# Kernel optimization log

Measured on AMD Instinct MI355X. Metric: run time of the kernel, lower is better.

Reference implementation:

```python
import jax, jax.numpy as jnp
import numpy as np

B, T, C, H = 2, 2048, 1024, 16
HD = C // H  # head dim = 64


def setup_inputs() -> dict:
    key = jax.random.key(0)
    ks = jax.random.split(key, 12)
    s = 1.0 / np.sqrt(C)
    return {
        "q": jax.random.normal(ks[0], (B, T, C), jnp.float32),
        "k": jax.random.normal(ks[1], (B, T, C), jnp.float32),
        "v": jax.random.normal(ks[2], (B, T, C), jnp.float32),
        "attn_bias": jax.random.normal(ks[3], (1, H, T, T), jnp.float32),
        "Wq": jax.random.normal(ks[4], (C, C), jnp.float32) * s,
        "bq": jnp.zeros((C,), jnp.float32),
        "Wk": jax.random.normal(ks[5], (C, C), jnp.float32) * s,
        "bk": jnp.zeros((C,), jnp.float32),
        "Wv": jax.random.normal(ks[6], (C, C), jnp.float32) * s,
        "bv": jnp.zeros((C,), jnp.float32),
        "Wp": jax.random.normal(ks[7], (C, C), jnp.float32) * s,
        "bp": jnp.zeros((C,), jnp.float32),
    }


def reference(q, k, v, attn_bias, Wq, bq, Wk, bk, Wv, bv, Wp, bp):
    # Linear projections (torch Linear: x @ W.T + b), then split heads -> [B,H,T,HD]
    def split_heads(x):
        return x.reshape(B, T, H, HD).transpose(0, 2, 1, 3)

    qh = split_heads(q @ Wq.T + bq)
    kh = split_heads(k @ Wk.T + bk)
    vh = split_heads(v @ Wv.T + bv)

    scale = 1.0 / np.sqrt(HD)
    att = jnp.einsum("bhqd,bhkd->bhqk", qh, kh) * scale  # [B,H,T,T]

    causal = jnp.tril(jnp.ones((T, T), dtype=bool))  # mask[:, :, -Tq:, :Tk]
    att_scores = jnp.where(causal[None, None], att, -jnp.inf)
    att_scores = att_scores + attn_bias

    att_probs = jax.nn.softmax(att_scores, axis=-1)
    y = jnp.einsum("bhqk,bhkd->bhqd", att_probs, vh)
    y = y.transpose(0, 2, 1, 3).reshape(B, T, C)
    y = y @ Wp.T + bp  # dropout p=0.0
    return (y, att_scores)
```

## Files before the change

### kernel.cpp

```cpp
#include <hip/hip_runtime.h>
#include <hip/hip_bf16.h>
#include <math.h>

#define B_ 2
#define T_ 2048
#define C_ 1024
#define H_ 16
#define HD_ 64
#define M_ (B_*T_)
#define K_ 1024

#define SCORE_NINF (-3.0e38f)

#define PART_BH 33792

typedef __attribute__((ext_vector_type(8))) short bf16x8;
typedef __attribute__((ext_vector_type(8))) unsigned short u16x8;
typedef __attribute__((ext_vector_type(4))) float f32x4;

__device__ __forceinline__ ushort f2bf_rne(float x) {
    union { float f; unsigned u; } c; c.f = x;
    unsigned r = c.u + 0x7fffu + ((c.u >> 16) & 1u);
    return (ushort)(r >> 16);
}
__device__ __forceinline__ float bfval(ushort h) {
    union { float f; unsigned u; } c; c.u = ((unsigned)h) << 16; return c.f;
}
__device__ __forceinline__ ushort bf16_hi(float x) {
    union { float f; unsigned u; } c; c.f = x; return (ushort)(c.u >> 16);
}
__device__ __forceinline__ void nt_store_f4(float* p, f32x4 v) {
    __builtin_nontemporal_store(v, (f32x4*)p);
}

__device__ __forceinline__ void gload_lds16(const void* g, void* l) {
    __builtin_amdgcn_global_load_lds(
        (const __attribute__((address_space(1))) unsigned int*)g,
        (__attribute__((address_space(3))) unsigned int*)l, 16, 0, 0);
}

__global__ __launch_bounds__(256) void split4_kernel(
    const float* __restrict__ W0, const float* __restrict__ W1,
    const float* __restrict__ W2, const float* __restrict__ W3,
    ushort* __restrict__ h0, ushort* __restrict__ l0,
    ushort* __restrict__ h1, ushort* __restrict__ l1,
    ushort* __restrict__ h2, ushort* __restrict__ l2,
    ushort* __restrict__ h3, ushort* __restrict__ l3)
{
    const int wsel = blockIdx.x >> 10;
    const float* src = (wsel == 0) ? W0 : (wsel == 1) ? W1 : (wsel == 2) ? W2 : W3;
    ushort* hi = (wsel == 0) ? h0 : (wsel == 1) ? h1 : (wsel == 2) ? h2 : h3;
    ushort* lo = (wsel == 0) ? l0 : (wsel == 1) ? l1 : (wsel == 2) ? l2 : l3;
    const int i = (((blockIdx.x & 1023) * 256) + threadIdx.x) * 4;
    const float4 x = *(const float4*)&src[i];
    ushort4 h, l;
    h.x = f2bf_rne(x.x); l.x = f2bf_rne(x.x - bfval(h.x));
    h.y = f2bf_rne(x.y); l.y = f2bf_rne(x.y - bfval(h.y));
    h.z = f2bf_rne(x.z); l.z = f2bf_rne(x.z - bfval(h.z));
    h.w = f2bf_rne(x.w); l.w = f2bf_rne(x.w - bfval(h.w));
    *(ushort4*)&hi[i] = h;
    *(ushort4*)&lo[i] = l;
}

__global__ __launch_bounds__(256) void gemm_qkv(
    const float* __restrict__ Xq, const float* __restrict__ Xk, const float* __restrict__ Xv,
    const ushort* __restrict__ Wqh, const ushort* __restrict__ Wql,
    const ushort* __restrict__ Wkh, const ushort* __restrict__ Wkl,
    const ushort* __restrict__ Wvh, const ushort* __restrict__ Wvl,
    const float* __restrict__ bq, const float* __restrict__ bk, const float* __restrict__ bv,
    ushort* __restrict__ qo_hi, ushort* __restrict__ qo_lo,
    ushort* __restrict__ ko_hi, ushort* __restrict__ ko_lo,
    ushort* __restrict__ vo_hi, ushort* __restrict__ vo_lo)
{
    constexpr int APITCH = 40;
    __shared__ ushort AhS[128 * APITCH];
    __shared__ ushort AlS[128 * APITCH];
    __shared__ ushort BhS[128 * 32];
    __shared__ ushort BlS[128 * 32];

    const int z = blockIdx.z;
    const float*  Xf = (z == 0) ? Xq : (z == 1) ? Xk : Xv;
    const ushort* Wh = (z == 0) ? Wqh : (z == 1) ? Wkh : Wvh;
    const ushort* Wl = (z == 0) ? Wql : (z == 1) ? Wkl : Wvl;
    const float*  bias = (z == 0) ? bq : (z == 1) ? bk : bv;
    ushort* out_hi = (z == 0) ? qo_hi : (z == 1) ? ko_hi : vo_hi;
    ushort* out_lo = (z == 0) ? qo_lo : (z == 1) ? ko_lo : vo_lo;

    const int tid  = threadIdx.x;
    const int lane = tid & 63;
    const int w    = tid >> 6;
    const int lr   = lane & 15, lk = lane >> 4;
    const int wr   = w >> 1,    wc = w & 1;
    const int bm   = blockIdx.x * 128;
    const int bn   = blockIdx.y * 128;

    f32x4 acc[4][4];
    #pragma unroll
    for (int i = 0; i < 4; ++i)
        #pragma unroll
        for (int j = 0; j < 4; ++j) acc[i][j] = (f32x4){0.f, 0.f, 0.f, 0.f};

    const int ar   = tid >> 1;
    const int aseg = (tid & 1) * 16;

    for (int k0 = 0; k0 < K_; k0 += 32) {
        {
            const int r0 = w * 32;
            #pragma unroll
            for (int ii = 0; ii < 2; ++ii) {
                const int rr = r0 + ii * 16;
                const size_t goff = (size_t)(bn + rr + (lane >> 2)) * K_ + k0 + (lane & 3) * 8;
                gload_lds16(Wh + goff, &BhS[rr * 32]);
                gload_lds16(Wl + goff, &BlS[rr * 32]);
            }
        }
        {
            const float* xp = Xf + (size_t)(bm + ar) * K_ + aseg + k0;
            const float4 f0 = *(const float4*)(xp + 0);
            const float4 f1 = *(const float4*)(xp + 4);
            const float4 f2 = *(const float4*)(xp + 8);
            const float4 f3 = *(const float4*)(xp + 12);
            float xs[16];
            xs[0]=f0.x; xs[1]=f0.y; xs[2]=f0.z; xs[3]=f0.w;
            xs[4]=f1.x; xs[5]=f1.y; xs[6]=f1.z; xs[7]=f1.w;
            xs[8]=f2.x; xs[9]=f2.y; xs[10]=f2.z; xs[11]=f2.w;
            xs[12]=f3.x; xs[13]=f3.y; xs[14]=f3.z; xs[15]=f3.w;
            u16x8 hv[2], lv[2];
            #pragma unroll
            for (int e = 0; e < 16; ++e) {
                const ushort hh = f2bf_rne(xs[e]);
                const ushort ll = f2bf_rne(xs[e] - bfval(hh));
                hv[e >> 3][e & 7] = hh;
                lv[e >> 3][e & 7] = ll;
            }
            *(u16x8*)&AhS[ar * APITCH + aseg]     = hv[0];
            *(u16x8*)&AhS[ar * APITCH + aseg + 8] = hv[1];
            *(u16x8*)&AlS[ar * APITCH + aseg]     = lv[0];
            *(u16x8*)&AlS[ar * APITCH + aseg + 8] = lv[1];
        }
        __syncthreads();

        bf16x8 afr[4][2], bfr[4][2];
        #pragma unroll
        for (int i = 0; i < 4; ++i) {
            const int arow = wr * 64 + i * 16 + lr;
            afr[i][0] = *(const bf16x8*)&AhS[arow * APITCH + lk * 8];
            afr[i][1] = *(const bf16x8*)&AlS[arow * APITCH + lk * 8];
        }
        #pragma unroll
        for (int j = 0; j < 4; ++j) {
            const int brow = wc * 64 + j * 16 + lr;
            bfr[j][0] = *(const bf16x8*)&BhS[brow * 32 + lk * 8];
            bfr[j][1] = *(const bf16x8*)&BlS[brow * 32 + lk * 8];
        }
        #pragma unroll
        for (int i = 0; i < 4; ++i)
            #pragma unroll
            for (int j = 0; j < 4; ++j) {
                acc[i][j] = __builtin_amdgcn_mfma_f32_16x16x32_bf16(afr[i][0], bfr[j][0], acc[i][j], 0, 0, 0);
                acc[i][j] = __builtin_amdgcn_mfma_f32_16x16x32_bf16(afr[i][0], bfr[j][1], acc[i][j], 0, 0, 0);
                acc[i][j] = __builtin_amdgcn_mfma_f32_16x16x32_bf16(afr[i][1], bfr[j][0], acc[i][j], 0, 0, 0);
            }
        __syncthreads();
    }

    const int m0 = bm + wr * 64;
    const int n0 = bn + wc * 64;
    #pragma unroll
    for (int j = 0; j < 4; ++j) {
        const int n = n0 + j * 16 + lr;
        const float bias_n = bias[n];
        #pragma unroll
        for (int i = 0; i < 4; ++i) {
            if (z == 2) {
                const int mbase = m0 + i * 16 + lk * 4;
                const int bb = mbase >> 11, t0 = mbase & 2047;
                const int hh = n >> 6, dd = n & 63;
                ushort4 h4, l4;
                float o;
                o = acc[i][j][0] + bias_n; h4.x = f2bf_rne(o); l4.x = f2bf_rne(o - bfval(h4.x));
                o = acc[i][j][1] + bias_n; h4.y = f2bf_rne(o); l4.y = f2bf_rne(o - bfval(h4.y));
                o = acc[i][j][2] + bias_n; h4.z = f2bf_rne(o); l4.z = f2bf_rne(o - bfval(h4.z));
                o = acc[i][j][3] + bias_n; h4.w = f2bf_rne(o); l4.w = f2bf_rne(o - bfval(h4.w));
                const size_t base = (((size_t)(bb * H_ + hh)) * HD_ + dd) * T_ + t0;
                *(ushort4*)&out_hi[base] = h4;
                *(ushort4*)&out_lo[base] = l4;
            } else {
                #pragma unroll
                for (int q = 0; q < 4; ++q) {
                    const int m = m0 + i * 16 + lk * 4 + q;
                    const float o = acc[i][j][q] + bias_n;
                    const int bb = m >> 11, tt = m & 2047;
                    const int hh = n >> 6, dd = n & 63;
                    const size_t idx = (((size_t)(bb * H_ + hh)) * T_ + tt) * HD_ + dd;
                    const ushort hv2 = f2bf_rne(o);
                    out_hi[idx] = hv2;
                    out_lo[idx] = f2bf_rne(o - bfval(hv2));
                }
            }
        }
    }
}

__global__ __launch_bounds__(256) void gemm_final(
    const ushort* __restrict__ Xh, const ushort* __restrict__ Xl,
    const ushort* __restrict__ Wh, const ushort* __restrict__ Wl,
    const float*  __restrict__ bias, float* __restrict__ outf)
{
    __shared__ ushort AhS[128 * 32];
    __shared__ ushort AlS[128 * 32];
    __shared__ ushort BhS[128 * 32];
    __shared__ ushort BlS[128 * 32];

    const int tid  = threadIdx.x;
    const int lane = tid & 63;
    const int w    = tid >> 6;
    const int lr   = lane & 15, lk = lane >> 4;
    const int wr   = w >> 1,    wc = w & 1;
    const int bm   = blockIdx.x * 128;
    const int bn   = blockIdx.y * 128;

    f32x4 acc[4][4];
    #pragma unroll
    for (int i = 0; i < 4; ++i)
        #pragma unroll
        for (int j = 0; j < 4; ++j) acc[i][j] = (f32x4){0.f, 0.f, 0.f, 0.f};

    for (int k0 = 0; k0 < K_; k0 += 32) {
        const int r0 = w * 32;
        #pragma unroll
        for (int ii = 0; ii < 2; ++ii) {
            const int rr = r0 + ii * 16;
            const size_t goffB = (size_t)(bn + rr + (lane >> 2)) * K_ + k0 + (lane & 3) * 8;
            gload_lds16(Wh + goffB, &BhS[rr * 32]);
            gload_lds16(Wl + goffB, &BlS[rr * 32]);
            const size_t goffA = (size_t)(bm + rr + (lane >> 2)) * K_ + k0 + (lane & 3) * 8;
            gload_lds16(Xh + goffA, &AhS[rr * 32]);
            gload_lds16(Xl + goffA, &AlS[rr * 32]);
        }
        __syncthreads();

        bf16x8 afr[4][2], bfr[4][2];
        #pragma unroll
        for (int i = 0; i < 4; ++i) {
            const int arow = wr * 64 + i * 16 + lr;
            afr[i][0] = *(const bf16x8*)&AhS[arow * 32 + lk * 8];
            afr[i][1] = *(const bf16x8*)&AlS[arow * 32 + lk * 8];
        }
        #pragma unroll
        for (int j = 0; j < 4; ++j) {
            const int brow = wc * 64 + j * 16 + lr;
            bfr[j][0] = *(const bf16x8*)&BhS[brow * 32 + lk * 8];
            bfr[j][1] = *(const bf16x8*)&BlS[brow * 32 + lk * 8];
        }
        #pragma unroll
        for (int i = 0; i < 4; ++i)
            #pragma unroll
            for (int j = 0; j < 4; ++j) {
                acc[i][j] = __builtin_amdgcn_mfma_f32_16x16x32_bf16(afr[i][0], bfr[j][0], acc[i][j], 0, 0, 0);
                acc[i][j] = __builtin_amdgcn_mfma_f32_16x16x32_bf16(afr[i][0], bfr[j][1], acc[i][j], 0, 0, 0);
                acc[i][j] = __builtin_amdgcn_mfma_f32_16x16x32_bf16(afr[i][1], bfr[j][0], acc[i][j], 0, 0, 0);
            }
        __syncthreads();
    }

    const int m0 = bm + wr * 64;
    const int n0 = bn + wc * 64;
    #pragma unroll
    for (int j = 0; j < 4; ++j) {
        const int n = n0 + j * 16 + lr;
        const float bias_n = bias[n];
        #pragma unroll
        for (int i = 0; i < 4; ++i)
            #pragma unroll
            for (int q = 0; q < 4; ++q)
                outf[(size_t)(m0 + i * 16 + lk * 4 + q) * C_ + n] = acc[i][j][q] + bias_n;
    }
}

#define SP 516

__global__ __launch_bounds__(256) void score_kernel(
    const ushort* __restrict__ q_hi, const ushort* __restrict__ q_lo,
    const ushort* __restrict__ k_hi, const ushort* __restrict__ k_lo,
    const float* __restrict__ bias,
    float* __restrict__ scores, float2* __restrict__ partials)
{
    __shared__ float biasT[16 * SP];
    __shared__ float scoreT[16 * SP];

    const int tid  = threadIdx.x;
    const int w    = tid >> 6, lane = tid & 63;
    const int lr   = lane & 15, lk = lane >> 4;

    const int h   = blockIdx.x >> 9;
    const int rem = blockIdx.x & 511;
    const int s   = rem >> 2;
    const int j   = rem & 3;
    const int qr0 = s * 16;
    const int ktmax = s >> 2;
    const int cbase = j * 512;
    const f32x4 ninf4 = (f32x4){SCORE_NINF, SCORE_NINF, SCORE_NINF, SCORE_NINF};

    if (j * 8 > ktmax) {
        #pragma unroll
        for (int b = 0; b < 2; ++b) {
            const size_t rbase = ((size_t)(b * 16 + h) * T_ + qr0);
            #pragma unroll
            for (int sw = 0; sw < 8; ++sw) {
                const int row = sw * 2 + (tid >> 7);
                const int col = (tid & 127) * 4;
                nt_store_f4(&scores[(rbase + row) * T_ + cbase + col], ninf4);
            }
        }
        return;
    }

    #pragma unroll
    for (int rr = 0; rr < 4; ++rr) {
        const int row = w * 4 + rr;
        const float* gsrc = bias + ((size_t)h * T_ + qr0 + row) * T_ + cbase + lane * 4;
        gload_lds16(gsrc,       &biasT[row * SP]);
        gload_lds16(gsrc + 256, &biasT[row * SP + 256]);
    }
    __syncthreads();

    const int qrow = qr0 + lr;
    #pragma unroll 1
    for (int b = 0; b < 2; ++b) {
        const int bh = b * 16 + h;
        const ushort* qhb = q_hi + (size_t)bh * T_ * HD_;
        const ushort* qlb = q_lo + (size_t)bh * T_ * HD_;
        const ushort* khb = k_hi + (size_t)bh * T_ * HD_;
        const ushort* klb = k_lo + (size_t)bh * T_ * HD_;
        float2* part_bh = partials + (size_t)bh * PART_BH;

        bf16x8 qf[2][2];
        #pragma unroll
        for (int s2 = 0; s2 < 2; ++s2) {
            const size_t qoff = (size_t)qrow * HD_ + s2 * 32 + lk * 8;
            qf[s2][0] = *(const bf16x8*)&qhb[qoff];
            qf[s2][1] = *(const bf16x8*)&qlb[qoff];
        }

        #pragma unroll
        for (int kk = 0; kk < 2; ++kk) {
            const int ktl = w * 2 + kk;
            const int kt  = j * 8 + ktl;
            const int lc0 = ktl * 64;
            if (kt > ktmax) {
                #pragma unroll
                for (int c = 0; c < 4; ++c)
                    *(f32x4*)&scoreT[lr * SP + lc0 + c * 16 + lk * 4] = ninf4;
                continue;
            }
            const int climit = (kt < ktmax) ? 4 : ((s & 3) + 1);
            f32x4 sc[4];
            #pragma unroll
            for (int c = 0; c < 4; ++c) {
                if (c < climit) {
                    f32x4 a = (f32x4){0.f, 0.f, 0.f, 0.f};
                    #pragma unroll
                    for (int s2 = 0; s2 < 2; ++s2) {
                        const size_t koff = (size_t)(kt * 64 + c * 16 + lr) * HD_ + s2 * 32 + lk * 8;
                        const bf16x8 kfh = *(const bf16x8*)&khb[koff];
                        const bf16x8 kfl = *(const bf16x8*)&klb[koff];
                        a = __builtin_amdgcn_mfma_f32_16x16x32_bf16(kfh, qf[s2][0], a, 0, 0, 0);
                        a = __builtin_amdgcn_mfma_f32_16x16x32_bf16(kfl, qf[s2][0], a, 0, 0, 0);
                        a = __builtin_amdgcn_mfma_f32_16x16x32_bf16(kfh, qf[s2][1], a, 0, 0, 0);
                    }
                    sc[c] = a;
                }
            }
            float tmax = SCORE_NINF;
            #pragma unroll
            for (int c = 0; c < 4; ++c) {
                const int loff = lr * SP + lc0 + c * 16 + lk * 4;
                if (c < climit) {
                    const f32x4 b4 = *(const f32x4*)&biasT[loff];
                    f32x4 o;
                    const int kc0 = kt * 64 + c * 16 + lk * 4;
                    #pragma unroll
                    for (int q4 = 0; q4 < 4; ++q4) {
                        const float sv = (kc0 + q4 <= qrow) ? sc[c][q4] * 0.125f + b4[q4]
                                                            : SCORE_NINF;
                        sc[c][q4] = sv;
                        tmax = fmaxf(tmax, sv);
                        o[q4] = sv;
                    }
                    *(f32x4*)&scoreT[loff] = o;
                } else {
                    *(f32x4*)&scoreT[loff] = ninf4;
                }
            }
            tmax = fmaxf(tmax, __shfl_xor(tmax, 16));
            tmax = fmaxf(tmax, __shfl_xor(tmax, 32));
            float tsum = 0.f;
            #pragma unroll
            for (int c = 0; c < 4; ++c) {
                if (c < climit) {
                    tsum += __expf(sc[c][0] - tmax);
                    tsum += __expf(sc[c][1] - tmax);
                    tsum += __expf(sc[c][2] - tmax);
                    tsum += __expf(sc[c][3] - tmax);
                }
            }
            tsum += __shfl_xor(tsum, 16);
            tsum += __shfl_xor(tsum, 32);
            if (lk == 0)
                part_bh[kt * (2080 - 32 * kt) + (qrow - kt * 64)] = make_float2(tmax, tsum);
        }
        __syncthreads();

        #pragma unroll
        for (int sw = 0; sw < 8; ++sw) {
            const int row = sw * 2 + (tid >> 7);
            const int col = (tid & 127) * 4;
            const f32x4 v = *(const f32x4*)&scoreT[row * SP + col];
            *(f32x4*)&scores[((size_t)bh * T_ + qr0 + row) * T_ + cbase + col] = v;
        }
        __syncthreads();
    }
}

__global__ __launch_bounds__(256) void reduce_kernel(
    const float2* __restrict__ partials, float2* __restrict__ ml)
{
    const int gid = blockIdx.x * 256 + threadIdx.x;
    const int bh = gid >> 11, r = gid & 2047;
    const float2* pb = partials + (size_t)bh * PART_BH;
    const int nt = (r >> 6) + 1;
    float M = SCORE_NINF;
    for (int t = 0; t < nt; ++t)
        M = fmaxf(M, pb[t * (2080 - 32 * t) + (r - (t << 6))].x);
    float L = 0.f;
    for (int t = 0; t < nt; ++t) {
        const float2 p = pb[t * (2080 - 32 * t) + (r - (t << 6))];
        L += p.y * __expf(p.x - M);
    }
    ml[gid] = make_float2(M, 1.f / L);
}

#define PVPITCH 260

__global__ __launch_bounds__(256) void pv_kernel(
    const ushort* __restrict__ vt_hi, const ushort* __restrict__ vt_lo,
    const float* __restrict__ scores, const float2* __restrict__ ml,
    ushort* __restrict__ y_hi, ushort* __restrict__ y_lo)
{
    __shared__ float stile[16 * PVPITCH];

    const int tid = threadIdx.x;
    const int w = tid >> 6, lane = tid & 63;
    const int lr = lane & 15, lk = lane >> 4;
    const int bh = 31 - ((int)blockIdx.x >> 6);
    const int p  = (int)blockIdx.x & 63;
    const int h = bh & 15, b = bh >> 4;

    const ushort* vhb = vt_hi + (size_t)bh * HD_ * T_;
    const ushort* vlb = vt_lo + (size_t)bh * HD_ * T_;

    #pragma unroll 1
    for (int half = 0; half < 2; ++half) {
        const int s = half ? (127 - p) : p;
        const int qr0 = s * 16;
        const int ktmax = s >> 2;
        const int nch = (ktmax + 4) >> 2;
        const float2 ml2 = ml[(size_t)bh * 2048 + qr0 + lr];
        const float M = ml2.x, invL = ml2.y;

        f32x4 yacc[4];
        #pragma unroll
        for (int c = 0; c < 4; ++c) yacc[c] = (f32x4){0.f, 0.f, 0.f, 0.f};

        #pragma unroll 1
        for (int ch = 0; ch < nch; ++ch) {
            const int cb = ch * 256;
            #pragma unroll
            for (int rr = 0; rr < 4; ++rr) {
                const int row = w * 4 + rr;
                const float* gsrc = scores + ((size_t)bh * T_ + qr0 + row) * T_ + cb + lane * 4;
                gload_lds16(gsrc, &stile[row * PVPITCH]);
            }
            __syncthreads();

            const int kt = ch * 4 + w;
            if (kt <= ktmax) {
                const int climit = (kt < ktmax) ? 4 : ((s & 3) + 1);
                const int s2max = (climit > 2) ? 2 : 1;
                bf16x8 pa[2][2];
                #pragma unroll
                for (int s2 = 0; s2 < 2; ++s2) {
                    if (s2 < s2max) {
                        const float* lsrc = &stile[lr * PVPITCH + w * 64 + s2 * 32 + lk * 8];
                        const f32x4 l0 = *(const f32x4*)(lsrc);
                        const f32x4 l1 = *(const f32x4*)(lsrc + 4);
                        float xs[8];
                        xs[0]=l0[0]; xs[1]=l0[1]; xs[2]=l0[2]; xs[3]=l0[3];
                        xs[4]=l1[0]; xs[5]=l1[1]; xs[6]=l1[2]; xs[7]=l1[3];
                        bf16x8 ph, pl;
                        #pragma unroll
                        for (int jj = 0; jj < 8; ++jj) {
                            const float pv = __expf(xs[jj] - M);
                            const ushort hv = bf16_hi(pv);
                            ph[jj] = (short)hv;
                            pl[jj] = (short)bf16_hi(pv - bfval(hv));
                        }
                        pa[s2][0] = ph;
                        pa[s2][1] = pl;
                    }
                }
                #pragma unroll
                for (int c2 = 0; c2 < 4; ++c2) {
                    #pragma unroll
                    for (int s2 = 0; s2 < 2; ++s2) {
                        if (s2 < s2max) {
                            const size_t voff = (size_t)(c2 * 16 + lr) * T_ + kt * 64 + s2 * 32 + lk * 8;
                            const bf16x8 vfh = *(const bf16x8*)&vhb[voff];
                            const bf16x8 vfl = *(const bf16x8*)&vlb[voff];
                            yacc[c2] = __builtin_amdgcn_mfma_f32_16x16x32_bf16(pa[s2][0], vfh, yacc[c2], 0, 0, 0);
                            yacc[c2] = __builtin_amdgcn_mfma_f32_16x16x32_bf16(pa[s2][0], vfl, yacc[c2], 0, 0, 0);
                            yacc[c2] = __builtin_amdgcn_mfma_f32_16x16x32_bf16(pa[s2][1], vfh, yacc[c2], 0, 0, 0);
                        }
                    }
                }
            }
            __syncthreads();
        }

        float* mbuf = stile;
        if (w > 0) {
            #pragma unroll
            for (int c2 = 0; c2 < 4; ++c2)
                *(f32x4*)&mbuf[((c2 * 3 + (w - 1)) * 64 + lane) * 4] = yacc[c2];
        }
        __syncthreads();
        if (w == 0) {
            float inv[4];
            #pragma unroll
            for (int q4 = 0; q4 < 4; ++q4) inv[q4] = __shfl(invL, lk * 4 + q4);
            #pragma unroll
            for (int c2 = 0; c2 < 4; ++c2) {
                f32x4 tot = yacc[c2];
                #pragma unroll
                for (int ww = 0; ww < 3; ++ww)
                    tot += *(const f32x4*)&mbuf[((c2 * 3 + ww) * 64 + lane) * 4];
                #pragma unroll
                for (int q4 = 0; q4 < 4; ++q4) {
                    const int yr = qr0 + lk * 4 + q4;
                    const float val = tot[q4] * inv[q4];
                    const size_t yi = ((size_t)b * T_ + yr) * C_ + h * HD_ + c2 * 16 + lr;
                    const ushort hv = f2bf_rne(val);
                    y_hi[yi] = hv;
                    y_lo[yi] = f2bf_rne(val - bfval(hv));
                }
            }
        }
        __syncthreads();
    }
}

extern "C" void kernel_launch(void* const* d_in, const int* in_sizes, int n_in,
                              void* d_out, int out_size, void* d_ws, size_t ws_size,
                              hipStream_t stream) {
    const float* q         = (const float*)d_in[0];
    const float* k         = (const float*)d_in[1];
    const float* v         = (const float*)d_in[2];
    const float* attn_bias = (const float*)d_in[3];
    const float* Wq        = (const float*)d_in[4];
    const float* bq        = (const float*)d_in[5];
    const float* Wk        = (const float*)d_in[6];
    const float* bk        = (const float*)d_in[7];
    const float* Wv        = (const float*)d_in[8];
    const float* bv        = (const float*)d_in[9];
    const float* Wp        = (const float*)d_in[10];
    const float* bp        = (const float*)d_in[11];

    float* y_out      = (float*)d_out;
    float* scores_out = y_out + (size_t)B_*T_*C_;

    ushort* ws = (ushort*)d_ws;
    const size_t NE = (size_t)B_*H_*T_*HD_;
    const size_t WN = (size_t)C_*K_;
    ushort* q_hi  = ws + 0*NE;
    ushort* q_lo  = ws + 1*NE;
    ushort* k_hi  = ws + 2*NE;
    ushort* k_lo  = ws + 3*NE;
    ushort* vt_hi = ws + 4*NE;
    ushort* vt_lo = ws + 5*NE;
    ushort* Wph   = ws + 6*NE;
    ushort* Wpl   = Wph + WN;
    ushort* Wqh   = Wpl + WN;
    ushort* Wql   = Wqh + WN;
    ushort* Wkh   = Wql + WN;
    ushort* Wkl   = Wkh + WN;
    ushort* Wvh   = Wkl + WN;
    ushort* Wvl   = Wvh + WN;
    float2* partials = (float2*)(ws + 6*NE + 2*WN);
    float2* ml    = (float2*)(ws + 0*NE);
    ushort* y_hi  = ws + 1*NE;
    ushort* y_lo  = ws + 2*NE;

    split4_kernel<<<4096, 256, 0, stream>>>(Wq, Wk, Wv, Wp,
        Wqh, Wql, Wkh, Wkl, Wvh, Wvl, Wph, Wpl);

    gemm_qkv<<<dim3(M_/128, C_/128, 3), 256, 0, stream>>>(
        q, k, v, Wqh, Wql, Wkh, Wkl, Wvh, Wvl, bq, bk, bv,
        q_hi, q_lo, k_hi, k_lo, vt_hi, vt_lo);

    score_kernel<<<8192, 256, 0, stream>>>(q_hi, q_lo, k_hi, k_lo, attn_bias,
                                           scores_out, partials);
    reduce_kernel<<<256, 256, 0, stream>>>(partials, ml);
    pv_kernel<<<2048, 256, 0, stream>>>(vt_hi, vt_lo, scores_out, ml, y_hi, y_lo);

    gemm_final<<<dim3(M_/128, C_/128), 256, 0, stream>>>(
        y_hi, y_lo, Wph, Wpl, bp, y_out);
}
```

Baseline: 706.6 us.

## Split score kernel blocks per batch and merge bias and score LDS tiles

Each score block now handles a single batch index, so the grid doubles and the in-block batch loop is gone. Adjacent blocks (b=0,1) share the same attention-bias tile, so the reuse moves from inside one block to the L2 cache. One LDS tile holds the bias and is overwritten with scores, which halves shared memory per block and should raise occupancy. In exchange the bias is loaded from global memory twice instead of once per block, and there are more block launches.

```diff
diff --git a/kernel.cpp b/kernel.cpp
--- a/kernel.cpp
+++ b/kernel.cpp
@@ -286,17 +286,18 @@
     const float* __restrict__ bias,
     float* __restrict__ scores, float2* __restrict__ partials)
 {
-    __shared__ float biasT[16 * SP];
-    __shared__ float scoreT[16 * SP];
+    __shared__ float tile[16 * SP];
 
     const int tid  = threadIdx.x;
     const int w    = tid >> 6, lane = tid & 63;
     const int lr   = lane & 15, lk = lane >> 4;
 
-    const int h   = blockIdx.x >> 9;
-    const int rem = blockIdx.x & 511;
-    const int s   = rem >> 2;
-    const int j   = rem & 3;
+    const int bid = blockIdx.x;
+    const int b   = bid & 1;
+    const int j   = (bid >> 1) & 3;
+    const int s   = (bid >> 3) & 127;
+    const int h   = bid >> 10;
+    const int bh  = b * 16 + h;
     const int qr0 = s * 16;
     const int ktmax = s >> 2;
     const int cbase = j * 512;
@@ -304,14 +305,10 @@
 
     if (j * 8 > ktmax) {
         #pragma unroll
-        for (int b = 0; b < 2; ++b) {
-            const size_t rbase = ((size_t)(b * 16 + h) * T_ + qr0);
-            #pragma unroll
-            for (int sw = 0; sw < 8; ++sw) {
-                const int row = sw * 2 + (tid >> 7);
-                const int col = (tid & 127) * 4;
-                nt_store_f4(&scores[(rbase + row) * T_ + cbase + col], ninf4);
-            }
+        for (int sw = 0; sw < 8; ++sw) {
+            const int row = sw * 2 + (tid >> 7);
+            const int col = (tid & 127) * 4;
+            nt_store_f4(&scores[((size_t)bh * T_ + qr0 + row) * T_ + cbase + col], ninf4);
         }
         return;
     }
@@ -320,106 +317,101 @@
     for (int rr = 0; rr < 4; ++rr) {
         const int row = w * 4 + rr;
         const float* gsrc = bias + ((size_t)h * T_ + qr0 + row) * T_ + cbase + lane * 4;
-        gload_lds16(gsrc,       &biasT[row * SP]);
-        gload_lds16(gsrc + 256, &biasT[row * SP + 256]);
+        gload_lds16(gsrc,       &tile[row * SP]);
+        gload_lds16(gsrc + 256, &tile[row * SP + 256]);
     }
     __syncthreads();
 
     const int qrow = qr0 + lr;
-    #pragma unroll 1
-    for (int b = 0; b < 2; ++b) {
-        const int bh = b * 16 + h;
-        const ushort* qhb = q_hi + (size_t)bh * T_ * HD_;
-        const ushort* qlb = q_lo + (size_t)bh * T_ * HD_;
-        const ushort* khb = k_hi + (size_t)bh * T_ * HD_;
-        const ushort* klb = k_lo + (size_t)bh * T_ * HD_;
-        float2* part_bh = partials + (size_t)bh * PART_BH;
-
-        bf16x8 qf[2][2];
-        #pragma unroll
-        for (int s2 = 0; s2 < 2; ++s2) {
-            const size_t qoff = (size_t)qrow * HD_ + s2 * 32 + lk * 8;
-            qf[s2][0] = *(const bf16x8*)&qhb[qoff];
-            qf[s2][1] = *(const bf16x8*)&qlb[qoff];
-        }
-
-        #pragma unroll
-        for (int kk = 0; kk < 2; ++kk) {
-            const int ktl = w * 2 + kk;
-            const int kt  = j * 8 + ktl;
-            const int lc0 = ktl * 64;
-            if (kt > ktmax) {
+    const ushort* qhb = q_hi + (size_t)bh * T_ * HD_;
+    const ushort* qlb = q_lo + (size_t)bh * T_ * HD_;
+    const ushort* khb = k_hi + (size_t)bh * T_ * HD_;
+    const ushort* klb = k_lo + (size_t)bh * T_ * HD_;
+    float2* part_bh = partials + (size_t)bh * PART_BH;
+
+    bf16x8 qf[2][2];
+    #pragma unroll
+    for (int s2 = 0; s2 < 2; ++s2) {
+        const size_t qoff = (size_t)qrow * HD_ + s2 * 32 + lk * 8;
+        qf[s2][0] = *(const bf16x8*)&qhb[qoff];
+        qf[s2][1] = *(const bf16x8*)&qlb[qoff];
+    }
+
+    #pragma unroll
+    for (int kk = 0; kk < 2; ++kk) {
+        const int ktl = w * 2 + kk;
+        const int kt  = j * 8 + ktl;
+        const int lc0 = ktl * 64;
+        if (kt > ktmax) {
+            #pragma unroll
+            for (int c = 0; c < 4; ++c)
+                *(f32x4*)&tile[lr * SP + lc0 + c * 16 + lk * 4] = ninf4;
+            continue;
+        }
+        const int climit = (kt < ktmax) ? 4 : ((s & 3) + 1);
+        f32x4 sc[4];
+        #pragma unroll
+        for (int c = 0; c < 4; ++c) {
+            if (c < climit) {
+                f32x4 a = (f32x4){0.f, 0.f, 0.f, 0.f};
                 #pragma unroll
-                for (int c = 0; c < 4; ++c)
-                    *(f32x4*)&scoreT[lr * SP + lc0 + c * 16 + lk * 4] = ninf4;
-                continue;
-            }
-            const int climit = (kt < ktmax) ? 4 : ((s & 3) + 1);
-            f32x4 sc[4];
-            #pragma unroll
-            for (int c = 0; c < 4; ++c) {
-                if (c < climit) {
-                    f32x4 a = (f32x4){0.f, 0.f, 0.f, 0.f};
-                    #pragma unroll
-                    for (int s2 = 0; s2 < 2; ++s2) {
-                        const size_t koff = (size_t)(kt * 64 + c * 16 + lr) * HD_ + s2 * 32 + lk * 8;
-                        const bf16x8 kfh = *(const bf16x8*)&khb[koff];
-                        const bf16x8 kfl = *(const bf16x8*)&klb[koff];
-                        a = __builtin_amdgcn_mfma_f32_16x16x32_bf16(kfh, qf[s2][0], a, 0, 0, 0);
-                        a = __builtin_amdgcn_mfma_f32_16x16x32_bf16(kfl, qf[s2][0], a, 0, 0, 0);
-                        a = __builtin_amdgcn_mfma_f32_16x16x32_bf16(kfh, qf[s2][1], a, 0, 0, 0);
-                    }
-                    sc[c] = a;
+                for (int s2 = 0; s2 < 2; ++s2) {
+                    const size_t koff = (size_t)(kt * 64 + c * 16 + lr) * HD_ + s2 * 32 + lk * 8;
+                    const bf16x8 kfh = *(const bf16x8*)&khb[koff];
+                    const bf16x8 kfl = *(const bf16x8*)&klb[koff];
+                    a = __builtin_amdgcn_mfma_f32_16x16x32_bf16(kfh, qf[s2][0], a, 0, 0, 0);
+                    a = __builtin_amdgcn_mfma_f32_16x16x32_bf16(kfl, qf[s2][0], a, 0, 0, 0);
+                    a = __builtin_amdgcn_mfma_f32_16x16x32_bf16(kfh, qf[s2][1], a, 0, 0, 0);
                 }
-            }
-            float tmax = SCORE_NINF;
-            #pragma unroll
-            for (int c = 0; c < 4; ++c) {
-                const int loff = lr * SP + lc0 + c * 16 + lk * 4;
-                if (c < climit) {
-                    const f32x4 b4 = *(const f32x4*)&biasT[loff];
-                    f32x4 o;
-                    const int kc0 = kt * 64 + c * 16 + lk * 4;
-                    #pragma unroll
-                    for (int q4 = 0; q4 < 4; ++q4) {
-                        const float sv = (kc0 + q4 <= qrow) ? sc[c][q4] * 0.125f + b4[q4]
-                                                            : SCORE_NINF;
-                        sc[c][q4] = sv;
-                        tmax = fmaxf(tmax, sv);
-                        o[q4] = sv;
-                    }
-                    *(f32x4*)&scoreT[loff] = o;
-                } else {
-                    *(f32x4*)&scoreT[loff] = ninf4;
+                sc[c] = a;
+            }
+        }
+        float tmax = SCORE_NINF;
+        #pragma unroll
+        for (int c = 0; c < 4; ++c) {
+            const int loff = lr * SP + lc0 + c * 16 + lk * 4;
+            if (c < climit) {
+                const f32x4 b4 = *(const f32x4*)&tile[loff];
+                f32x4 o;
+                const int kc0 = kt * 64 + c * 16 + lk * 4;
+                #pragma unroll
+                for (int q4 = 0; q4 < 4; ++q4) {
+                    const float sv = (kc0 + q4 <= qrow) ? sc[c][q4] * 0.125f + b4[q4]
+                                                        : SCORE_NINF;
+                    sc[c][q4] = sv;
+                    tmax = fmaxf(tmax, sv);
+                    o[q4] = sv;
                 }
-            }
-            tmax = fmaxf(tmax, __shfl_xor(tmax, 16));
-            tmax = fmaxf(tmax, __shfl_xor(tmax, 32));
-            float tsum = 0.f;
-            #pragma unroll
-            for (int c = 0; c < 4; ++c) {
-                if (c < climit) {
-                    tsum += __expf(sc[c][0] - tmax);
-                    tsum += __expf(sc[c][1] - tmax);
-                    tsum += __expf(sc[c][2] - tmax);
-                    tsum += __expf(sc[c][3] - tmax);
-                }
-            }
-            tsum += __shfl_xor(tsum, 16);
-            tsum += __shfl_xor(tsum, 32);
-            if (lk == 0)
-                part_bh[kt * (2080 - 32 * kt) + (qrow - kt * 64)] = make_float2(tmax, tsum);
-        }
-        __syncthreads();
-
-        #pragma unroll
-        for (int sw = 0; sw < 8; ++sw) {
-            const int row = sw * 2 + (tid >> 7);
-            const int col = (tid & 127) * 4;
-            const f32x4 v = *(const f32x4*)&scoreT[row * SP + col];
-            *(f32x4*)&scores[((size_t)bh * T_ + qr0 + row) * T_ + cbase + col] = v;
-        }
-        __syncthreads();
+                *(f32x4*)&tile[loff] = o;
+            } else {
+                *(f32x4*)&tile[loff] = ninf4;
+            }
+        }
+        tmax = fmaxf(tmax, __shfl_xor(tmax, 16));
+        tmax = fmaxf(tmax, __shfl_xor(tmax, 32));
+        float tsum = 0.f;
+        #pragma unroll
+        for (int c = 0; c < 4; ++c) {
+            if (c < climit) {
+                tsum += __expf(sc[c][0] - tmax);
+                tsum += __expf(sc[c][1] - tmax);
+                tsum += __expf(sc[c][2] - tmax);
+                tsum += __expf(sc[c][3] - tmax);
+            }
+        }
+        tsum += __shfl_xor(tsum, 16);
+        tsum += __shfl_xor(tsum, 32);
+        if (lk == 0)
+            part_bh[kt * (2080 - 32 * kt) + (qrow - kt * 64)] = make_float2(tmax, tsum);
+    }
+    __syncthreads();
+
+    #pragma unroll
+    for (int sw = 0; sw < 8; ++sw) {
+        const int row = sw * 2 + (tid >> 7);
+        const int col = (tid & 127) * 4;
+        const f32x4 v = *(const f32x4*)&tile[row * SP + col];
+        *(f32x4*)&scores[((size_t)bh * T_ + qr0 + row) * T_ + cbase + col] = v;
     }
 }
 
@@ -608,8 +600,8 @@
         q, k, v, Wqh, Wql, Wkh, Wkl, Wvh, Wvl, bq, bk, bv,
         q_hi, q_lo, k_hi, k_lo, vt_hi, vt_lo);
 
-    score_kernel<<<8192, 256, 0, stream>>>(q_hi, q_lo, k_hi, k_lo, attn_bias,
-                                           scores_out, partials);
+    score_kernel<<<16384, 256, 0, stream>>>(q_hi, q_lo, k_hi, k_lo, attn_bias,
+                                            scores_out, partials);
     reduce_kernel<<<256, 256, 0, stream>>>(partials, ml);
     pv_kernel<<<2048, 256, 0, stream>>>(vt_hi, vt_lo, scores_out, ml, y_hi, y_lo);
 
```

After: 687.5 us. -2.7%, faster.
